# Kernel tuning notes

Measured on AMD Instinct MI355X. Metric: run time of the kernel, lower is better.

The kernel has to match this reference:

```python
import jax, jax.numpy as jnp
import numpy as np

T, B, E, H, D, K = 4096, 8, 1024, 8, 128, 64  # K = proj_dim; phi dim = 2K
CHUNK = 128
TAU = 1.0
EPS = 1e-6


def setup_inputs() -> dict:
    key = jax.random.key(0)
    k = jax.random.split(key, 8)
    gain = 1.0 / np.sqrt(2.0)
    a = gain * np.sqrt(6.0 / (E + E))  # xavier_uniform bound with gain 1/sqrt(2)
    def lin_w(kk):
        return jax.random.uniform(kk, (E, E), jnp.float32, -a, a)
    return {
        "x": jax.random.normal(k[0], (T, B, E), jnp.float32),
        "random_matrices": jax.random.normal(k[1], (H, K, D), jnp.float32),
        "Wq": lin_w(k[2]), "bq": jnp.zeros((E,), jnp.float32),
        "Wk": lin_w(k[3]), "bk": jnp.zeros((E,), jnp.float32),
        "Wv": lin_w(k[4]), "bv": jnp.zeros((E,), jnp.float32),
        "Wo": lin_w(k[5]), "bo": jnp.zeros((E,), jnp.float32),
        "sigma": jnp.ones((H, 1, D), jnp.float32),
    }


def _causal_rfa(pq, pk, v):
    # pq/pk: [T,B,H,2K], v: [T,B,H,D]. Chunked linear-attention recurrence:
    # s_t = sum_{i<=t} phi_k_i (x) v_i ; z_t = sum_{i<=t} phi_k_i ; out = (q.s)/(q.z)
    t, b, h, k2 = pq.shape
    d = v.shape[-1]
    nc = t // CHUNK
    pq_c = pq.reshape(nc, CHUNK, b, h, k2)
    pk_c = pk.reshape(nc, CHUNK, b, h, k2)
    v_c = v.reshape(nc, CHUNK, b, h, d)
    mask = jnp.tril(jnp.ones((CHUNK, CHUNK), pq.dtype))  # inclusive causal (i <= t)

    def step(carry, inp):
        s, z = carry  # [B,H,2K,D], [B,H,2K]
        cq, ck, cv = inp  # [C,B,H,2K] x2, [C,B,H,D]
        scores = jnp.einsum('tbhk,sbhk->bhts', cq, ck) * mask[None, None]
        num = (jnp.einsum('bhts,sbhd->tbhd', scores, cv)
               + jnp.einsum('tbhk,bhkd->tbhd', cq, s))
        den = (jnp.transpose(scores.sum(-1), (2, 0, 1))
               + jnp.einsum('tbhk,bhk->tbh', cq, z))
        out = num / jnp.maximum(den, EPS)[..., None]
        s = s + jnp.einsum('sbhk,sbhd->bhkd', ck, cv)
        z = z + ck.sum(0)
        return (s, z), out

    s0 = jnp.zeros((b, h, k2, d), pq.dtype)
    z0 = jnp.zeros((b, h, k2), pq.dtype)
    _, outs = jax.lax.scan(step, (s0, z0), (pq_c, pk_c, v_c))
    return outs.reshape(t, b, h * d)


def reference(x, random_matrices, Wq, bq, Wk, bk, Wv, bv, Wo, bo, sigma):
    t, b, e = x.shape
    q = (x @ Wq.T + bq).reshape(t, b, H, D)
    kk = (x @ Wk.T + bk).reshape(t, b, H, D)
    v = (x @ Wv.T + bv).reshape(t, b, H, D)
    rm = (sigma * random_matrices) / TAU  # reparam projection, [H,K,D]

    def phi(u):
        # scale by d^{-1/4} (softmax temperature split between q and k)
        p = jnp.einsum('tbhd,hkd->tbhk', u * (D ** -0.25), rm)
        return jnp.concatenate([jnp.sin(p), jnp.cos(p)], axis=-1) * (K ** -0.5)

    attn = _causal_rfa(phi(q), phi(kk), v)  # [T,B,E]
    return attn @ Wo.T + bo
```

## Files before the change

### kernel.cpp

```cpp
#include <hip/hip_runtime.h>
#include <math.h>

#define TT 4096
#define BB 8
#define EE 1024
#define HH 8
#define DD 128
#define KK 64
#define PHI2 128
#define NPROJ 512
#define CH 128
#define NC 32
#define NROWS 32768
#define EPSV 1e-6f

typedef float f32x4 __attribute__((ext_vector_type(4)));
typedef __bf16 bf16x8 __attribute__((ext_vector_type(8)));
typedef unsigned short u16x8 __attribute__((ext_vector_type(8)));
typedef unsigned short u16x4 __attribute__((ext_vector_type(4)));

__device__ __forceinline__ unsigned short f2b(float f) {
  union { float f; unsigned int u; } v; v.f = f;
  unsigned int u = v.u;
  u += 0x7fffu + ((u >> 16) & 1u);
  return (unsigned short)(u >> 16);
}
__device__ __forceinline__ float b2f(unsigned short h) {
  union { float f; unsigned int u; } v; v.u = ((unsigned int)h) << 16;
  return v.f;
}
__device__ __forceinline__ void fast_sc(float x, float& s, float& c) {
  s = __sinf(x); c = __cosf(x);
}

__device__ __forceinline__ void stage16(const void* g, void* l) {
  __builtin_amdgcn_global_load_lds(
      (const __attribute__((address_space(1))) void*)g,
      (__attribute__((address_space(3))) void*)l, 16, 0, 0);
}

__device__ __forceinline__ bf16x8 ldfrag(const unsigned short* p) {
  u16x8 s = *(const u16x8*)p;
  return __builtin_bit_cast(bf16x8, s);
}
__device__ __forceinline__ bf16x8 ldfrag64(const unsigned short* p) {
  u16x4 a = *(const u16x4*)p;
  u16x4 b = *(const u16x4*)(p + 4);
  u16x8 v = {a[0], a[1], a[2], a[3], b[0], b[1], b[2], b[3]};
  return __builtin_bit_cast(bf16x8, v);
}

__device__ __forceinline__ void stage_rs(const unsigned short* gbase, size_t rstride,
                                         unsigned short* lds, int tid)
{
  int r = tid >> 1, c0 = (tid & 1) * 16;
  const unsigned short* gp = gbase + (size_t)r * rstride + c0;
  u16x8 v0 = *(const u16x8*)gp;
  u16x8 v1 = *(const u16x8*)(gp + 8);
  *(u16x8*)(lds + r * 40 + c0) = v0;
  *(u16x8*)(lds + r * 40 + c0 + 8) = v1;
}

__global__ __launch_bounds__(256) void split_kernel(
    const float* __restrict__ in, unsigned short* __restrict__ hi,
    unsigned short* __restrict__ lo, int n4)
{
  int stride = gridDim.x * 256;
  for (int i = blockIdx.x * 256 + threadIdx.x; i < n4; i += stride) {
    float4 v = ((const float4*)in)[i];
    ushort4 h, l;
    h.x = f2b(v.x); l.x = f2b(v.x - b2f(h.x));
    h.y = f2b(v.y); l.y = f2b(v.y - b2f(h.y));
    h.z = f2b(v.z); l.z = f2b(v.z - b2f(h.z));
    h.w = f2b(v.w); l.w = f2b(v.w - b2f(h.w));
    ((ushort4*)hi)[i] = h;
    ((ushort4*)lo)[i] = l;
  }
}

__global__ __launch_bounds__(256) void weff_kernel(
    const float* __restrict__ rmat, const float* __restrict__ sigma,
    const float* __restrict__ W, const float* __restrict__ bvec,
    float* __restrict__ Weff, float* __restrict__ beff)
{
  __shared__ float rme[64][130];
  __shared__ float Wt[128][130];
  const int et = blockIdx.x;
  const int h  = blockIdx.y;
  const int tid = threadIdx.x;
  const int e0 = et * 128;
  const float s4 = 0.29730177875068026f;

  for (int f = tid; f < 64 * 32; f += 256) {
    int kk = f >> 5, d = (f & 31) * 4;
    float4 rv = *(const float4*)(rmat + ((size_t)(h * 64 + kk)) * 128 + d);
    const float* sg = sigma + h * 128 + d;
    rme[kk][d + 0] = rv.x * sg[0] * s4;
    rme[kk][d + 1] = rv.y * sg[1] * s4;
    rme[kk][d + 2] = rv.z * sg[2] * s4;
    rme[kk][d + 3] = rv.w * sg[3] * s4;
  }
  for (int f = tid; f < 128 * 32; f += 256) {
    int dd = f >> 5, e = (f & 31) * 4;
    *(float4*)&Wt[dd][e] = *(const float4*)(W + ((size_t)(h * 128 + dd)) * EE + e0 + e);
  }
  __syncthreads();
  const int nl = tid >> 2;
  const int el0 = (tid & 3) * 32;
  for (int e = 0; e < 32; ++e) {
    float acc = 0.f;
#pragma unroll
    for (int d = 0; d < 128; ++d)
      acc = fmaf(rme[nl][d], Wt[d][el0 + e], acc);
    Weff[(size_t)(h * 64 + nl) * EE + e0 + el0 + e] = acc;
  }
  if (et == 0 && tid < 64) {
    float acc = 0.f;
    for (int d = 0; d < 128; ++d)
      acc = fmaf(rme[tid][d], bvec[h * 128 + d], acc);
    beff[h * 64 + tid] = acc;
  }
}

template<int OUTBF16, int NPASS>
__global__ __launch_bounds__(256) void gemm_mfma(
    const unsigned short* __restrict__ Ahi, const unsigned short* __restrict__ Alo,
    const unsigned short* __restrict__ Whi, const unsigned short* __restrict__ Wlo,
    const float* __restrict__ bias, void* __restrict__ Cout, int M, int N, int Kd)
{
  __shared__ __align__(16) unsigned short Ahs[128 * 32];
  __shared__ __align__(16) unsigned short Whs[128 * 32];
  __shared__ __align__(16) unsigned short Wls[128 * 32];
  __shared__ __align__(16) unsigned short Als[NPASS == 3 ? 128 * 32 : 8];
  const int tid = threadIdx.x;
  const int w = tid >> 6, l = tid & 63;
  int bx, by;
  {
    int id = blockIdx.x + gridDim.x * blockIdx.y;
    int xcd = id & 7, k = id >> 3;
    by = k % gridDim.y;
    bx = xcd * (gridDim.x >> 3) + k / gridDim.y;
  }
  const int m0 = bx * 128, n0 = by * 128;
  const int wm = (w >> 1) * 64, wn = (w & 1) * 64;
  const int rowA = tid >> 2, ko = (tid & 3) * 8;

  f32x4 acc[4][4] = {};
  const int sb0 = w * 512, sb1 = 2048 + w * 512;
  const int fA = (wm + (l & 15)) * 32 + (l >> 4) * 8;
  const int fW = (wn + (l & 15)) * 32 + (l >> 4) * 8;

  const unsigned short* gah0 = Ahi + (size_t)(m0 + rowA) * Kd + ko;
  const unsigned short* gah1 = Ahi + (size_t)(m0 + 64 + rowA) * Kd + ko;
  const unsigned short* gwh0 = Whi + (size_t)(n0 + rowA) * Kd + ko;
  const unsigned short* gwh1 = Whi + (size_t)(n0 + 64 + rowA) * Kd + ko;
  const unsigned short* gwl0 = Wlo + (size_t)(n0 + rowA) * Kd + ko;
  const unsigned short* gwl1 = Wlo + (size_t)(n0 + 64 + rowA) * Kd + ko;
  const unsigned short* gal0 = nullptr;
  const unsigned short* gal1 = nullptr;
  if (NPASS == 3) {
    gal0 = Alo + (size_t)(m0 + rowA) * Kd + ko;
    gal1 = Alo + (size_t)(m0 + 64 + rowA) * Kd + ko;
  }

#pragma unroll 1
  for (int kt = 0; kt < Kd; kt += 32) {
    __syncthreads();
    stage16(gah0 + kt, Ahs + sb0);
    stage16(gah1 + kt, Ahs + sb1);
    stage16(gwh0 + kt, Whs + sb0);
    stage16(gwh1 + kt, Whs + sb1);
    stage16(gwl0 + kt, Wls + sb0);
    stage16(gwl1 + kt, Wls + sb1);
    if (NPASS == 3) {
      stage16(gal0 + kt, Als + sb0);
      stage16(gal1 + kt, Als + sb1);
    }
    __syncthreads();
    bf16x8 ah[4], wh[4], wl[4];
#pragma unroll
    for (int i = 0; i < 4; ++i) {
      ah[i] = ldfrag(Ahs + fA + i * 512);
      wh[i] = ldfrag(Whs + fW + i * 512);
      wl[i] = ldfrag(Wls + fW + i * 512);
    }
#pragma unroll
    for (int i = 0; i < 4; ++i)
#pragma unroll
      for (int j = 0; j < 4; ++j)
        acc[i][j] = __builtin_amdgcn_mfma_f32_16x16x32_bf16(ah[i], wh[j], acc[i][j], 0, 0, 0);
#pragma unroll
    for (int i = 0; i < 4; ++i)
#pragma unroll
      for (int j = 0; j < 4; ++j)
        acc[i][j] = __builtin_amdgcn_mfma_f32_16x16x32_bf16(ah[i], wl[j], acc[i][j], 0, 0, 0);
    if (NPASS == 3) {
      bf16x8 al[4];
#pragma unroll
      for (int i = 0; i < 4; ++i) al[i] = ldfrag(Als + fA + i * 512);
#pragma unroll
      for (int i = 0; i < 4; ++i)
#pragma unroll
        for (int j = 0; j < 4; ++j)
          acc[i][j] = __builtin_amdgcn_mfma_f32_16x16x32_bf16(al[i], wh[j], acc[i][j], 0, 0, 0);
    }
  }

  const int cl = l & 15, rg = (l >> 4) * 4;
  float bvv[4];
#pragma unroll
  for (int j = 0; j < 4; ++j) bvv[j] = bias[n0 + wn + j * 16 + cl];
#pragma unroll
  for (int i = 0; i < 4; ++i) {
    const int row = m0 + wm + i * 16 + rg;
#pragma unroll
    for (int r = 0; r < 4; ++r) {
#pragma unroll
      for (int j = 0; j < 4; ++j) {
        float v = acc[i][j][r] + bvv[j];
        if (OUTBF16) {
          ((unsigned short*)Cout)[(size_t)(row + r) * N + n0 + wn + j * 16 + cl] = f2b(v);
        } else {
          ((float*)Cout)[(size_t)(row + r) * N + n0 + wn + j * 16 + cl] = v;
        }
      }
    }
  }
}

__global__ __launch_bounds__(256) void vtrans_kernel(
    const unsigned short* __restrict__ Vb, unsigned short* __restrict__ VbT)
{
  __shared__ __align__(16) unsigned short T[128 * 132];
  const int tt = blockIdx.x, b = blockIdx.y, h = blockIdx.z;
  const int tid = threadIdx.x;
  {
    int t = tid >> 1, f0 = (tid & 1) * 64;
    const unsigned short* gp = Vb + ((size_t)((tt * 128 + t) * BB + b)) * EE + h * DD + f0;
    unsigned short* lp = T + t * 132 + f0;
#pragma unroll
    for (int k8 = 0; k8 < 8; ++k8) {
      u16x8 v = *(const u16x8*)(gp + k8 * 8);
      u16x4 vl = __builtin_shufflevector(v, v, 0, 1, 2, 3);
      u16x4 vh = __builtin_shufflevector(v, v, 4, 5, 6, 7);
      *(u16x4*)(lp + k8 * 8) = vl;
      *(u16x4*)(lp + k8 * 8 + 4) = vh;
    }
  }
  __syncthreads();
  const size_t obase = ((size_t)(b * HH + h) * DD) * 4096 + tt * 128;
#pragma unroll
  for (int dd = 0; dd < 4; ++dd) {
    int d = (tid >> 3) + dd * 32;
    int t0 = (tid & 7) * 16;
    u16x8 o0, o1;
#pragma unroll
    for (int e = 0; e < 8; ++e) {
      o0[e] = T[(t0 + e) * 132 + d];
      o1[e] = T[(t0 + 8 + e) * 132 + d];
    }
    *(u16x8*)(VbT + obase + (size_t)d * 4096 + t0) = o0;
    *(u16x8*)(VbT + obase + (size_t)d * 4096 + t0 + 8) = o1;
  }
}

__global__ __launch_bounds__(256) void den1_kernel(
    const float* __restrict__ Pk, float* __restrict__ Z1)
{
  __shared__ float red[4][130];
  const int c = blockIdx.x, b = blockIdx.y, h = blockIdx.z;
  const int tid = threadIdx.x;
  const int k = tid & 63, part = tid >> 6;
  float ss = 0.f, cs = 0.f;
  const float* pb = Pk + ((size_t)(c * CH) * BB + b) * NPROJ + h * KK + k;
  for (int j = part * 32; j < part * 32 + 32; ++j) {
    float p = pb[(size_t)j * BB * NPROJ];
    float sv, cv; fast_sc(p, sv, cv);
    ss += sv; cs += cv;
  }
  red[part][k] = ss * 0.125f;
  red[part][k + 65] = cs * 0.125f;
  __syncthreads();
  if (tid < 128) {
    int f = tid;
    int idx = (f < 64) ? f : (f + 1);
    float s = red[0][idx] + red[1][idx] + red[2][idx] + red[3][idx];
    Z1[((size_t)(b * HH + h) * NC + c) * 128 + f] = s;
  }
}

__global__ __launch_bounds__(256) void zscan_kernel(float* __restrict__ Z1)
{
  int gid = blockIdx.x * 256 + threadIdx.x;
  if (gid >= 64 * 128) return;
  int bh = gid >> 7, f = gid & 127;
  float* p = Z1 + (size_t)bh * NC * 128 + f;
  float run = 0.f;
#pragma unroll
  for (int cc = 0; cc < NC; ++cc) {
    float t = p[cc * 128];
    p[cc * 128] = run;
    run += t;
  }
}

__global__ __launch_bounds__(256) void den2_kernel(
    const float* __restrict__ Pq, const float* __restrict__ Pk,
    const float* __restrict__ Z1, float* __restrict__ Den,
    unsigned short* __restrict__ Phq, unsigned short* __restrict__ Phk)
{
  __shared__ float Ks[128][132];
  const int c = blockIdx.x, b = blockIdx.y, h = blockIdx.z;
  const int tid = threadIdx.x;
  const int bh = b * HH + h;
  {
    int j = tid >> 1, k0 = (tid & 1) * 32;
    const float* pp = Pk + ((size_t)(c * CH + j) * BB + b) * NPROJ + h * KK + k0;
#pragma unroll
    for (int k4 = 0; k4 < 32; k4 += 4) {
      float4 p = *(const float4*)(pp + k4);
      float sv, cv;
      fast_sc(p.x, sv, cv); Ks[j][k0 + k4 + 0] = sv * 0.125f; Ks[j][64 + k0 + k4 + 0] = cv * 0.125f;
      fast_sc(p.y, sv, cv); Ks[j][k0 + k4 + 1] = sv * 0.125f; Ks[j][64 + k0 + k4 + 1] = cv * 0.125f;
      fast_sc(p.z, sv, cv); Ks[j][k0 + k4 + 2] = sv * 0.125f; Ks[j][64 + k0 + k4 + 2] = cv * 0.125f;
      fast_sc(p.w, sv, cv); Ks[j][k0 + k4 + 3] = sv * 0.125f; Ks[j][64 + k0 + k4 + 3] = cv * 0.125f;
    }
  }
  __syncthreads();
  {
#pragma unroll
    for (int it = 0; it < 8; ++it) {
      int row = (tid >> 4) + it * 16;
      int ch8 = tid & 15;
      f32x4 a = *(const f32x4*)&Ks[row][ch8 * 8];
      f32x4 bb = *(const f32x4*)&Ks[row][ch8 * 8 + 4];
      u16x8 o;
      o[0] = f2b(a[0]); o[1] = f2b(a[1]); o[2] = f2b(a[2]); o[3] = f2b(a[3]);
      o[4] = f2b(bb[0]); o[5] = f2b(bb[1]); o[6] = f2b(bb[2]); o[7] = f2b(bb[3]);
      *(u16x8*)(Phk + ((size_t)(c * CH + row) * BB + b) * EE + h * PHI2 + ch8 * 8) = o;
    }
  }
  __syncthreads();
  if (tid < 128) {
    int f = tid;
    float run = Z1[((size_t)bh * NC + c) * 128 + f];
    for (int j = 0; j < 128; ++j) { run += Ks[j][f]; Ks[j][f] = run; }
  }
  __syncthreads();
  {
    int row = tid >> 1, half = tid & 1;
    const float* pq = Pq + ((size_t)(c * CH + row) * BB + b) * NPROJ + h * KK;
    float accd = 0.f;
#pragma unroll
    for (int k8 = 0; k8 < 8; ++k8) {
      float4 p0 = *(const float4*)(pq + k8 * 8);
      float4 p1 = *(const float4*)(pq + k8 * 8 + 4);
      float ph[8];
      float sv, cv;
      fast_sc(p0.x, sv, cv); ph[0] = (half ? cv : sv) * 0.125f;
      fast_sc(p0.y, sv, cv); ph[1] = (half ? cv : sv) * 0.125f;
      fast_sc(p0.z, sv, cv); ph[2] = (half ? cv : sv) * 0.125f;
      fast_sc(p0.w, sv, cv); ph[3] = (half ? cv : sv) * 0.125f;
      fast_sc(p1.x, sv, cv); ph[4] = (half ? cv : sv) * 0.125f;
      fast_sc(p1.y, sv, cv); ph[5] = (half ? cv : sv) * 0.125f;
      fast_sc(p1.z, sv, cv); ph[6] = (half ? cv : sv) * 0.125f;
      fast_sc(p1.w, sv, cv); ph[7] = (half ? cv : sv) * 0.125f;
#pragma unroll
      for (int e = 0; e < 8; ++e)
        accd = fmaf(ph[e], Ks[row][half * 64 + k8 * 8 + e], accd);
      float* dst = &Ks[row][half * 64 + k8 * 4];
#pragma unroll
      for (int e2 = 0; e2 < 4; ++e2) {
        unsigned int pk = (unsigned int)f2b(ph[2 * e2]) |
                          ((unsigned int)f2b(ph[2 * e2 + 1]) << 16);
        dst[e2] = __builtin_bit_cast(float, pk);
      }
    }
    accd += __shfl_xor(accd, 1);
    if (half == 0) Den[(size_t)bh * TT + c * CH + row] = accd;
  }
  __syncthreads();
  {
#pragma unroll
    for (int it = 0; it < 8; ++it) {
      int row = (tid >> 4) + it * 16;
      int ch8 = tid & 15;
      int slot = (ch8 < 8) ? ch8 * 4 : 64 + (ch8 - 8) * 4;
      u16x8 o = __builtin_bit_cast(u16x8, *(const f32x4*)&Ks[row][slot]);
      *(u16x8*)(Phq + ((size_t)(c * CH + row) * BB + b) * EE + h * PHI2 + ch8 * 8) = o;
    }
  }
}

__global__ __launch_bounds__(256) void pass1_mfma(
    const unsigned short* __restrict__ Phk, const unsigned short* __restrict__ VbT,
    unsigned short* __restrict__ St)
{
  __shared__ __align__(16) unsigned short KT[128 * 132];
  __shared__ __align__(16) unsigned short Am[128 * 40];
  const int c = blockIdx.x, b = blockIdx.y, h = blockIdx.z;
  const int tid = threadIdx.x;
  const int w = tid >> 6, l = tid & 63;
  const int wm = (w >> 1) * 64, wn = (w & 1) * 64;
  const int cl = l & 15, ks = l >> 4;
  const int bh = b * HH + h;

  {
    int j = tid >> 1, f0 = (tid & 1) * 64;
    const unsigned short* gp = Phk + ((size_t)(c * CH + j) * BB + b) * EE + h * PHI2 + f0;
#pragma unroll
    for (int k8 = 0; k8 < 8; ++k8) {
      u16x8 v = *(const u16x8*)(gp + k8 * 8);
#pragma unroll
      for (int e = 0; e < 8; ++e) KT[(f0 + k8 * 8 + e) * 132 + j] = v[e];
    }
  }

  f32x4 acc[4][4] = {};
  const unsigned short* vbase = VbT + (size_t)bh * DD * 4096 + c * CH;
#pragma unroll 1
  for (int j0 = 0; j0 < 128; j0 += 32) {
    __syncthreads();
    stage_rs(vbase + j0, 4096, Am, tid);
    __syncthreads();
    bf16x8 af[4], wf[4];
#pragma unroll
    for (int i = 0; i < 4; ++i) {
      af[i] = ldfrag(Am + (wm + cl + i * 16) * 40 + ks * 8);
      wf[i] = ldfrag64(KT + (wn + cl + i * 16) * 132 + j0 + ks * 8);
    }
#pragma unroll
    for (int i = 0; i < 4; ++i)
#pragma unroll
      for (int j = 0; j < 4; ++j)
        acc[i][j] = __builtin_amdgcn_mfma_f32_16x16x32_bf16(af[i], wf[j], acc[i][j], 0, 0, 0);
  }
  unsigned short* sp = St + (size_t)(bh * NC + c) * (DD * PHI2);
#pragma unroll
  for (int i = 0; i < 4; ++i) {
    int d = wm + i * 16 + ks * 4;
#pragma unroll
    for (int r = 0; r < 4; ++r) {
#pragma unroll
      for (int j = 0; j < 4; ++j)
        sp[(size_t)(d + r) * PHI2 + wn + j * 16 + cl] = f2b(acc[i][j][r]);
    }
  }
}

__global__ __launch_bounds__(256) void sscan_kernel(unsigned short* __restrict__ Sb)
{
  int gid = blockIdx.x * 256 + threadIdx.x;
  if (gid >= 64 * CH * DD) return;
  int bh = gid >> 14, fd = gid & 16383;
  unsigned short* p = Sb + (size_t)bh * NC * 16384 + fd;
  float run = 0.f;
#pragma unroll
  for (int cc = 0; cc < NC; ++cc) {
    float t = b2f(p[(size_t)cc * 16384]);
    p[(size_t)cc * 16384] = f2b(run);
    run += t;
  }
}

__global__ __launch_bounds__(256) void attn_mfma(
    const unsigned short* __restrict__ Phq, const unsigned short* __restrict__ Phk,
    const unsigned short* __restrict__ VbT, const unsigned short* __restrict__ St,
    const float* __restrict__ Den, unsigned short* __restrict__ Ob)
{
  __shared__ __align__(16) unsigned short Qs[128 * 132];
  __shared__ __align__(16) unsigned short sc[128 * 132];
  __shared__ __align__(16) unsigned short Sm[128 * 40];
  __shared__ float den_s[128];
  const int c = blockIdx.x, b = blockIdx.y, h = blockIdx.z;
  const int tid = threadIdx.x;
  const int w = tid >> 6, l = tid & 63;
  const int wm = (w >> 1) * 64, wn = (w & 1) * 64;
  const int cl = l & 15, ks = l >> 4;
  const int bh = b * HH + h;

  {
    int r = tid >> 1, f0 = (tid & 1) * 64;
    const unsigned short* gp = Phq + ((size_t)(c * CH + r) * BB + b) * EE + h * PHI2 + f0;
    unsigned short* lp = Qs + r * 132 + f0;
#pragma unroll
    for (int k8 = 0; k8 < 8; ++k8) {
      u16x8 v = *(const u16x8*)(gp + k8 * 8);
      u16x4 vl = __builtin_shufflevector(v, v, 0, 1, 2, 3);
      u16x4 vh = __builtin_shufflevector(v, v, 4, 5, 6, 7);
      *(u16x4*)(lp + k8 * 8) = vl;
      *(u16x4*)(lp + k8 * 8 + 4) = vh;
    }
  }
  if (tid < 128) den_s[tid] = Den[(size_t)bh * TT + c * CH + tid];

  f32x4 acc[4][4] = {};
  const unsigned short* kbase = Phk + ((size_t)(c * CH) * BB + b) * EE + h * PHI2;
#pragma unroll 1
  for (int ft = 0; ft < PHI2; ft += 32) {
    __syncthreads();
    stage_rs(kbase + ft, (size_t)BB * EE, Sm, tid);
    __syncthreads();
    if (w != 1) {
      bf16x8 af[4], wf[4];
#pragma unroll
      for (int i = 0; i < 4; ++i) {
        af[i] = ldfrag64(Qs + (wm + cl + i * 16) * 132 + ft + ks * 8);
        wf[i] = ldfrag(Sm + (wn + cl + i * 16) * 40 + ks * 8);
      }
#pragma unroll
      for (int i = 0; i < 4; ++i)
#pragma unroll
        for (int j = 0; j < 4; ++j)
          acc[i][j] = __builtin_amdgcn_mfma_f32_16x16x32_bf16(af[i], wf[j], acc[i][j], 0, 0, 0);
    }
  }
  __syncthreads();
#pragma unroll
  for (int i = 0; i < 4; ++i) {
    int row0 = wm + i * 16 + ks * 4;
#pragma unroll
    for (int r = 0; r < 4; ++r) {
      int row = row0 + r;
#pragma unroll
      for (int j = 0; j < 4; ++j) {
        int col = wn + j * 16 + cl;
        sc[row * 132 + col] = f2b((col <= row) ? acc[i][j][r] : 0.f);
      }
    }
  }
  __syncthreads();

#pragma unroll
  for (int i = 0; i < 4; ++i)
#pragma unroll
    for (int j = 0; j < 4; ++j) acc[i][j] = (f32x4){0.f, 0.f, 0.f, 0.f};

  const unsigned short* vbase = VbT + (size_t)bh * DD * 4096 + c * CH;
#pragma unroll 1
  for (int j0 = 0; j0 < 128; j0 += 32) {
    __syncthreads();
    stage_rs(vbase + j0, 4096, Sm, tid);
    __syncthreads();
    if (!(wm == 0 && j0 >= 64)) {
      bf16x8 af[4], wf[4];
#pragma unroll
      for (int i = 0; i < 4; ++i) {
        af[i] = ldfrag64(sc + (wm + cl + i * 16) * 132 + j0 + ks * 8);
        wf[i] = ldfrag(Sm + (wn + cl + i * 16) * 40 + ks * 8);
      }
#pragma unroll
      for (int i = 0; i < 4; ++i)
#pragma unroll
        for (int j = 0; j < 4; ++j)
          acc[i][j] = __builtin_amdgcn_mfma_f32_16x16x32_bf16(af[i], wf[j], acc[i][j], 0, 0, 0);
    }
  }
  const unsigned short* sbase = St + (size_t)(bh * NC + c) * (DD * PHI2);
#pragma unroll 1
  for (int f0 = 0; f0 < PHI2; f0 += 32) {
    __syncthreads();
    stage_rs(sbase + f0, PHI2, Sm, tid);
    __syncthreads();
    bf16x8 af[4], wf[4];
#pragma unroll
    for (int i = 0; i < 4; ++i) {
      af[i] = ldfrag64(Qs + (wm + cl + i * 16) * 132 + f0 + ks * 8);
      wf[i] = ldfrag(Sm + (wn + cl + i * 16) * 40 + ks * 8);
    }
#pragma unroll
    for (int i = 0; i < 4; ++i)
#pragma unroll
      for (int j = 0; j < 4; ++j)
        acc[i][j] = __builtin_amdgcn_mfma_f32_16x16x32_bf16(af[i], wf[j], acc[i][j], 0, 0, 0);
  }
#pragma unroll
  for (int i = 0; i < 4; ++i) {
    int row0 = wm + i * 16 + ks * 4;
#pragma unroll
    for (int r = 0; r < 4; ++r) {
      int row = row0 + r;
      float inv = 1.0f / fmaxf(den_s[row], EPSV);
      unsigned short* op = Ob + ((size_t)(c * CH + row) * BB + b) * EE + h * DD;
#pragma unroll
      for (int j = 0; j < 4; ++j)
        op[wn + j * 16 + cl] = f2b(acc[i][j][r] * inv);
    }
  }
}

extern "C" void kernel_launch(void* const* d_in, const int* in_sizes, int n_in,
                              void* d_out, int out_size, void* d_ws, size_t ws_size,
                              hipStream_t stream)
{
  const float* x     = (const float*)d_in[0];
  const float* rmat  = (const float*)d_in[1];
  const float* Wq    = (const float*)d_in[2];
  const float* bq    = (const float*)d_in[3];
  const float* Wk    = (const float*)d_in[4];
  const float* bk    = (const float*)d_in[5];
  const float* Wv    = (const float*)d_in[6];
  const float* bv    = (const float*)d_in[7];
  const float* Wo    = (const float*)d_in[8];
  const float* bo    = (const float*)d_in[9];
  const float* sigma = (const float*)d_in[10];

  char* wsb = (char*)d_ws;
  float* pq_p = (float*)wsb;
  float* pk_p = (float*)(wsb + (64LL << 20));
  unsigned short* Stb = (unsigned short*)wsb;
  unsigned short* Ob  = (unsigned short*)(wsb + (64LL << 20));
  unsigned short* Vb  = (unsigned short*)(wsb + (128LL << 20));
  float* Z1  = (float*)(wsb + (128LL << 20));
  float* Den = (float*)(wsb + (129LL << 20));
  unsigned short* Woh = (unsigned short*)(wsb + (130LL << 20));
  unsigned short* Wol = (unsigned short*)(wsb + (132LL << 20));
  unsigned short* VbT = (unsigned short*)(wsb + (192LL << 20));
  float* Weq = (float*)(wsb + (240LL << 20));
  float* Wek = (float*)(wsb + (242LL << 20));
  float* beq = (float*)(wsb + (244LL << 20));
  float* bek = (float*)(wsb + (244LL << 20) + 65536);
  unsigned short* Weqh = (unsigned short*)(wsb + (245LL << 20));
  unsigned short* Weql = (unsigned short*)(wsb + (246LL << 20));
  unsigned short* Wekh = (unsigned short*)(wsb + (247LL << 20));
  unsigned short* Wekl = (unsigned short*)(wsb + (248LL << 20));
  unsigned short* Wvh  = (unsigned short*)(wsb + (249LL << 20));
  unsigned short* Wvl  = (unsigned short*)(wsb + (251LL << 20));

  char* ob = (char*)d_out;
  unsigned short* xhi = (unsigned short*)ob;
  unsigned short* xlo = (unsigned short*)(ob + (64LL << 20));
  unsigned short* Phq = (unsigned short*)ob;
  unsigned short* Phk = (unsigned short*)(ob + (64LL << 20));

  dim3 bt(256);
  hipLaunchKernelGGL(split_kernel, dim3(2048), bt, 0, stream, x, xhi, xlo, NROWS * EE / 4);
  hipLaunchKernelGGL(weff_kernel, dim3(8, 8), bt, 0, stream, rmat, sigma, Wq, bq, Weq, beq);
  hipLaunchKernelGGL(weff_kernel, dim3(8, 8), bt, 0, stream, rmat, sigma, Wk, bk, Wek, bek);
  hipLaunchKernelGGL(split_kernel, dim3(512), bt, 0, stream, Weq, Weqh, Weql, NPROJ * EE / 4);
  hipLaunchKernelGGL(split_kernel, dim3(512), bt, 0, stream, Wek, Wekh, Wekl, NPROJ * EE / 4);
  hipLaunchKernelGGL(split_kernel, dim3(1024), bt, 0, stream, Wv, Wvh, Wvl, EE * EE / 4);
  hipLaunchKernelGGL((gemm_mfma<0, 3>), dim3(NROWS / 128, NPROJ / 128), bt, 0, stream,
                     xhi, xlo, Weqh, Weql, beq, (void*)pq_p, NROWS, NPROJ, EE);
  hipLaunchKernelGGL((gemm_mfma<0, 3>), dim3(NROWS / 128, NPROJ / 128), bt, 0, stream,
                     xhi, xlo, Wekh, Wekl, bek, (void*)pk_p, NROWS, NPROJ, EE);
  hipLaunchKernelGGL((gemm_mfma<1, 2>), dim3(NROWS / 128, EE / 128), bt, 0, stream,
                     xhi, (const unsigned short*)0, Wvh, Wvl, bv, (void*)Vb, NROWS, EE, EE);
  hipLaunchKernelGGL(vtrans_kernel, dim3(NC, BB, HH), bt, 0, stream, Vb, VbT);
  hipLaunchKernelGGL(den1_kernel, dim3(NC, BB, HH), bt, 0, stream, pk_p, Z1);
  hipLaunchKernelGGL(zscan_kernel, dim3(32), bt, 0, stream, Z1);
  hipLaunchKernelGGL(den2_kernel, dim3(NC, BB, HH), bt, 0, stream, pq_p, pk_p, Z1, Den, Phq, Phk);
  hipLaunchKernelGGL(pass1_mfma, dim3(NC, BB, HH), bt, 0, stream, Phk, VbT, Stb);
  hipLaunchKernelGGL(sscan_kernel, dim3(4096), bt, 0, stream, Stb);
  hipLaunchKernelGGL(attn_mfma, dim3(NC, BB, HH), bt, 0, stream, Phq, Phk, VbT, Stb, Den, Ob);
  hipLaunchKernelGGL(split_kernel, dim3(1024), bt, 0, stream, Wo, Woh, Wol, EE * EE / 4);
  hipLaunchKernelGGL((gemm_mfma<0, 2>), dim3(NROWS / 128, EE / 128), bt, 0, stream,
                     Ob, (const unsigned short*)0, Woh, Wol, bo, (void*)d_out, NROWS, EE, EE);
}
```

Before: 1.183 ms.

## Fuse Q/K projection GEMMs and drop low-part weight pass for V and O

```diff
diff --git a/kernel.cpp b/kernel.cpp
--- a/kernel.cpp
+++ b/kernel.cpp
@@ -8,7 +8,7 @@
 #define DD 128
 #define KK 64
 #define PHI2 128
-#define NPROJ 512
+#define PSTR 1024
 #define CH 128
 #define NC 32
 #define NROWS 32768
@@ -130,8 +130,8 @@
 {
   __shared__ __align__(16) unsigned short Ahs[128 * 32];
   __shared__ __align__(16) unsigned short Whs[128 * 32];
-  __shared__ __align__(16) unsigned short Wls[128 * 32];
-  __shared__ __align__(16) unsigned short Als[NPASS == 3 ? 128 * 32 : 8];
+  __shared__ __align__(16) unsigned short Wls[(NPASS >= 2) ? 128 * 32 : 8];
+  __shared__ __align__(16) unsigned short Als[(NPASS == 3) ? 128 * 32 : 8];
   const int tid = threadIdx.x;
   const int w = tid >> 6, l = tid & 63;
   int bx, by;
@@ -154,8 +154,12 @@
   const unsigned short* gah1 = Ahi + (size_t)(m0 + 64 + rowA) * Kd + ko;
   const unsigned short* gwh0 = Whi + (size_t)(n0 + rowA) * Kd + ko;
   const unsigned short* gwh1 = Whi + (size_t)(n0 + 64 + rowA) * Kd + ko;
-  const unsigned short* gwl0 = Wlo + (size_t)(n0 + rowA) * Kd + ko;
-  const unsigned short* gwl1 = Wlo + (size_t)(n0 + 64 + rowA) * Kd + ko;
+  const unsigned short* gwl0 = nullptr;
+  const unsigned short* gwl1 = nullptr;
+  if (NPASS >= 2) {
+    gwl0 = Wlo + (size_t)(n0 + rowA) * Kd + ko;
+    gwl1 = Wlo + (size_t)(n0 + 64 + rowA) * Kd + ko;
+  }
   const unsigned short* gal0 = nullptr;
   const unsigned short* gal1 = nullptr;
   if (NPASS == 3) {
@@ -170,39 +174,48 @@
     stage16(gah1 + kt, Ahs + sb1);
     stage16(gwh0 + kt, Whs + sb0);
     stage16(gwh1 + kt, Whs + sb1);
-    stage16(gwl0 + kt, Wls + sb0);
-    stage16(gwl1 + kt, Wls + sb1);
+    if (NPASS >= 2) {
+      stage16(gwl0 + kt, Wls + sb0);
+      stage16(gwl1 + kt, Wls + sb1);
+    }
     if (NPASS == 3) {
       stage16(gal0 + kt, Als + sb0);
       stage16(gal1 + kt, Als + sb1);
     }
     __syncthreads();
-    bf16x8 ah[4], wh[4], wl[4];
+    bf16x8 ah[4], wh[4];
 #pragma unroll
     for (int i = 0; i < 4; ++i) {
       ah[i] = ldfrag(Ahs + fA + i * 512);
       wh[i] = ldfrag(Whs + fW + i * 512);
-      wl[i] = ldfrag(Wls + fW + i * 512);
     }
 #pragma unroll
     for (int i = 0; i < 4; ++i)
 #pragma unroll
       for (int j = 0; j < 4; ++j)
         acc[i][j] = __builtin_amdgcn_mfma_f32_16x16x32_bf16(ah[i], wh[j], acc[i][j], 0, 0, 0);
-#pragma unroll
-    for (int i = 0; i < 4; ++i)
-#pragma unroll
-      for (int j = 0; j < 4; ++j)
-        acc[i][j] = __builtin_amdgcn_mfma_f32_16x16x32_bf16(ah[i], wl[j], acc[i][j], 0, 0, 0);
+    if (NPASS >= 2) {
+      bf16x8 wl[4];
+#pragma unroll
+      for (int i = 0; i < 4; ++i) wl[i] = ldfrag(Wls + fW + i * 512);
+#pragma unroll
+      for (int i = 0; i < 4; ++i)
+#pragma unroll
+        for (int j = 0; j < 4; ++j)
+          acc[i][j] = __builtin_amdgcn_mfma_f32_16x16x32_bf16(ah[i], wl[j], acc[i][j], 0, 0, 0);
+    }
     if (NPASS == 3) {
-      bf16x8 al[4];
-#pragma unroll
-      for (int i = 0; i < 4; ++i) al[i] = ldfrag(Als + fA + i * 512);
+      bf16x8 al[4], whx[4];
+#pragma unroll
+      for (int i = 0; i < 4; ++i) {
+        al[i] = ldfrag(Als + fA + i * 512);
+        whx[i] = ldfrag(Whs + fW + i * 512);
+      }
 #pragma unroll
       for (int i = 0; i < 4; ++i)
 #pragma unroll
         for (int j = 0; j < 4; ++j)
-          acc[i][j] = __builtin_amdgcn_mfma_f32_16x16x32_bf16(al[i], wh[j], acc[i][j], 0, 0, 0);
+          acc[i][j] = __builtin_amdgcn_mfma_f32_16x16x32_bf16(al[i], whx[j], acc[i][j], 0, 0, 0);
     }
   }
 
@@ -272,9 +285,9 @@
   const int tid = threadIdx.x;
   const int k = tid & 63, part = tid >> 6;
   float ss = 0.f, cs = 0.f;
-  const float* pb = Pk + ((size_t)(c * CH) * BB + b) * NPROJ + h * KK + k;
+  const float* pb = Pk + ((size_t)(c * CH) * BB + b) * PSTR + h * KK + k;
   for (int j = part * 32; j < part * 32 + 32; ++j) {
-    float p = pb[(size_t)j * BB * NPROJ];
+    float p = pb[(size_t)j * BB * PSTR];
     float sv, cv; fast_sc(p, sv, cv);
     ss += sv; cs += cv;
   }
@@ -315,7 +328,7 @@
   const int bh = b * HH + h;
   {
     int j = tid >> 1, k0 = (tid & 1) * 32;
-    const float* pp = Pk + ((size_t)(c * CH + j) * BB + b) * NPROJ + h * KK + k0;
+    const float* pp = Pk + ((size_t)(c * CH + j) * BB + b) * PSTR + h * KK + k0;
 #pragma unroll
     for (int k4 = 0; k4 < 32; k4 += 4) {
       float4 p = *(const float4*)(pp + k4);
@@ -349,7 +362,7 @@
   __syncthreads();
   {
     int row = tid >> 1, half = tid & 1;
-    const float* pq = Pq + ((size_t)(c * CH + row) * BB + b) * NPROJ + h * KK;
+    const float* pq = Pq + ((size_t)(c * CH + row) * BB + b) * PSTR + h * KK;
     float accd = 0.f;
 #pragma unroll
     for (int k8 = 0; k8 < 8; ++k8) {
@@ -606,8 +619,9 @@
   const float* sigma = (const float*)d_in[10];
 
   char* wsb = (char*)d_ws;
-  float* pq_p = (float*)wsb;
-  float* pk_p = (float*)(wsb + (64LL << 20));
+  float* Pqk = (float*)wsb;
+  float* pq_p = Pqk;
+  float* pk_p = Pqk + 512;
   unsigned short* Stb = (unsigned short*)wsb;
   unsigned short* Ob  = (unsigned short*)(wsb + (64LL << 20));
   unsigned short* Vb  = (unsigned short*)(wsb + (128LL << 20));
@@ -616,14 +630,10 @@
   unsigned short* Woh = (unsigned short*)(wsb + (130LL << 20));
   unsigned short* Wol = (unsigned short*)(wsb + (132LL << 20));
   unsigned short* VbT = (unsigned short*)(wsb + (192LL << 20));
-  float* Weq = (float*)(wsb + (240LL << 20));
-  float* Wek = (float*)(wsb + (242LL << 20));
-  float* beq = (float*)(wsb + (244LL << 20));
-  float* bek = (float*)(wsb + (244LL << 20) + 65536);
-  unsigned short* Weqh = (unsigned short*)(wsb + (245LL << 20));
-  unsigned short* Weql = (unsigned short*)(wsb + (246LL << 20));
-  unsigned short* Wekh = (unsigned short*)(wsb + (247LL << 20));
-  unsigned short* Wekl = (unsigned short*)(wsb + (248LL << 20));
+  float* Weqk = (float*)(wsb + (240LL << 20));
+  float* beqk = (float*)(wsb + (244LL << 20));
+  unsigned short* Wqkh = (unsigned short*)(wsb + (245LL << 20));
+  unsigned short* Wqkl = (unsigned short*)(wsb + (247LL << 20));
   unsigned short* Wvh  = (unsigned short*)(wsb + (249LL << 20));
   unsigned short* Wvl  = (unsigned short*)(wsb + (251LL << 20));
 
@@ -635,17 +645,15 @@
 
   dim3 bt(256);
   hipLaunchKernelGGL(split_kernel, dim3(2048), bt, 0, stream, x, xhi, xlo, NROWS * EE / 4);
-  hipLaunchKernelGGL(weff_kernel, dim3(8, 8), bt, 0, stream, rmat, sigma, Wq, bq, Weq, beq);
-  hipLaunchKernelGGL(weff_kernel, dim3(8, 8), bt, 0, stream, rmat, sigma, Wk, bk, Wek, bek);
-  hipLaunchKernelGGL(split_kernel, dim3(512), bt, 0, stream, Weq, Weqh, Weql, NPROJ * EE / 4);
-  hipLaunchKernelGGL(split_kernel, dim3(512), bt, 0, stream, Wek, Wekh, Wekl, NPROJ * EE / 4);
+  hipLaunchKernelGGL(weff_kernel, dim3(8, 8), bt, 0, stream, rmat, sigma, Wq, bq, Weqk, beqk);
+  hipLaunchKernelGGL(weff_kernel, dim3(8, 8), bt, 0, stream, rmat, sigma, Wk, bk,
+                     Weqk + (size_t)512 * EE, beqk + 512);
+  hipLaunchKernelGGL(split_kernel, dim3(1024), bt, 0, stream, Weqk, Wqkh, Wqkl, 1024 * EE / 4);
   hipLaunchKernelGGL(split_kernel, dim3(1024), bt, 0, stream, Wv, Wvh, Wvl, EE * EE / 4);
-  hipLaunchKernelGGL((gemm_mfma<0, 3>), dim3(NROWS / 128, NPROJ / 128), bt, 0, stream,
-                     xhi, xlo, Weqh, Weql, beq, (void*)pq_p, NROWS, NPROJ, EE);
-  hipLaunchKernelGGL((gemm_mfma<0, 3>), dim3(NROWS / 128, NPROJ / 128), bt, 0, stream,
-                     xhi, xlo, Wekh, Wekl, bek, (void*)pk_p, NROWS, NPROJ, EE);
-  hipLaunchKernelGGL((gemm_mfma<1, 2>), dim3(NROWS / 128, EE / 128), bt, 0, stream,
-                     xhi, (const unsigned short*)0, Wvh, Wvl, bv, (void*)Vb, NROWS, EE, EE);
+  hipLaunchKernelGGL((gemm_mfma<0, 3>), dim3(NROWS / 128, 1024 / 128), bt, 0, stream,
+                     xhi, xlo, Wqkh, Wqkl, beqk, (void*)Pqk, NROWS, 1024, EE);
+  hipLaunchKernelGGL((gemm_mfma<1, 1>), dim3(NROWS / 128, EE / 128), bt, 0, stream,
+                     xhi, (const unsigned short*)0, Wvh, Wvh, bv, (void*)Vb, NROWS, EE, EE);
   hipLaunchKernelGGL(vtrans_kernel, dim3(NC, BB, HH), bt, 0, stream, Vb, VbT);
   hipLaunchKernelGGL(den1_kernel, dim3(NC, BB, HH), bt, 0, stream, pk_p, Z1);
   hipLaunchKernelGGL(zscan_kernel, dim3(32), bt, 0, stream, Z1);
@@ -654,6 +662,6 @@
   hipLaunchKernelGGL(sscan_kernel, dim3(4096), bt, 0, stream, Stb);
   hipLaunchKernelGGL(attn_mfma, dim3(NC, BB, HH), bt, 0, stream, Phq, Phk, VbT, Stb, Den, Ob);
   hipLaunchKernelGGL(split_kernel, dim3(1024), bt, 0, stream, Wo, Woh, Wol, EE * EE / 4);
-  hipLaunchKernelGGL((gemm_mfma<0, 2>), dim3(NROWS / 128, EE / 128), bt, 0, stream,
-                     Ob, (const unsigned short*)0, Woh, Wol, bo, (void*)d_out, NROWS, EE, EE);
-}
+  hipLaunchKernelGGL((gemm_mfma<0, 1>), dim3(NROWS / 128, EE / 128), bt, 0, stream,
+                     Ob, (const unsigned short*)0, Woh, Woh, bo, (void*)d_out, NROWS, EE, EE);
+}
```

Result: faster. 1.074 ms (-9.2%).
